# Performance work log

Measured on AMD Instinct MI355X. Metric: run time of the kernel, lower is better.

Reference implementation:

```python
import jax, jax.numpy as jnp
import numpy as np

MAX_M = 16
B, H, N_LEN = 16, 256, 4096


def _ref_dft_np(n, h):
    a = np.arange(n)
    M = np.exp(-2j * np.pi * np.outer(a, a) / n)  # (n, n) complex
    M = np.broadcast_to(M, (h, n, n))
    return np.ascontiguousarray(np.stack([M.real, M.imag], axis=-1)).astype(np.float32)


def setup_inputs() -> dict:
    key = jax.random.key(0)
    k1, k2 = jax.random.split(key)
    x_real = jax.random.normal(k1, (B, H, N_LEN), dtype=jnp.float32)
    x_imag = jax.random.normal(k2, (B, H, N_LEN), dtype=jnp.float32)
    # Learned DFT matrices are initialized to the exact reference DFT matrices
    # (learn_additive=False path in the torch module).
    return {
        "x_real": x_real,
        "x_imag": x_imag,
        "mat_2": jnp.asarray(_ref_dft_np(2, H)),
        "mat_4": jnp.asarray(_ref_dft_np(4, H)),
        "mat_8": jnp.asarray(_ref_dft_np(8, H)),
        "mat_16": jnp.asarray(_ref_dft_np(16, H)),
        "N": N_LEN,
    }


def _twiddle(n, m):
    na = jnp.arange(n)[:, None]
    ma = jnp.arange(m)[None, :]
    return jnp.exp((-2j * jnp.pi / (n * m)) * (na * ma).astype(jnp.float32))  # (n, m)


def _cooley_tukey(k, n, m, mats):
    # k: (..., n*m) complex; FFT of length n*m along last dim.
    k = k.reshape(k.shape[:-1] + (m, n))  # '... (m n) -> ... m n'
    # n m-length DFTs along rows: mats[m] is (H, m, m), broadcasts over leading dims.
    k_f = jnp.einsum('...mo,...on->...mn', mats[m], k)
    twi = _twiddle(n, m).astype(k_f.dtype)  # (n, m)
    k_f = jnp.einsum('nm,...mn->...nm', twi, k_f)  # transpose + twiddle
    if n <= MAX_M:
        k_f = jnp.einsum('...no,...om->...nm', mats[n], k_f)
    else:
        k_f = jnp.moveaxis(k_f, -1, -3)  # '... h n m -> ... m h n'
        k_f = _cooley_tukey(k_f, n // MAX_M, MAX_M, mats)
        k_f = jnp.moveaxis(k_f, -3, -1)  # '... m h n -> ... h n m'
    return k_f.reshape(k_f.shape[:-2] + (k_f.shape[-2] * k_f.shape[-1],))


def reference(x_real, x_imag, mat_2, mat_4, mat_8, mat_16, N):
    x = x_real + 1j * x_imag  # (B, H, N) complex64
    mats = {p: (mm[..., 0] + 1j * mm[..., 1])
            for p, mm in ((2, mat_2), (4, mat_4), (8, mat_8), (16, mat_16))}
    out = _cooley_tukey(x, N // MAX_M, MAX_M, mats)  # (B, H, N) complex
    # view_as_real representation of the complex FFT output
    return jnp.stack([out.real, out.imag], axis=-1)  # (B, H, N, 2)
```

## Files before the change

kernel.cpp:

```cpp
#include <hip/hip_runtime.h>
#include <stdint.h>

typedef _Float16 f16x8 __attribute__((ext_vector_type(8)));
typedef float    f32x4 __attribute__((ext_vector_type(4)));

union FragU { unsigned u[4]; f16x8 h; };

__device__ __forceinline__ unsigned pkh(float a, float b) {
    return __builtin_bit_cast(unsigned, __builtin_amdgcn_cvt_pkrtz(a, b));
}

#define MFMA(A, B, C) __builtin_amdgcn_mfma_f32_16x16x32_f16((A).h, (B).h, (C), 0, 0, 0)

#define K1 (-1.5339807878856412e-03f)
#define K2 (-2.4543692606170259e-02f)

__global__ __launch_bounds__(256) void fft4096_mfma(
    const float* __restrict__ xre, const float* __restrict__ xim,
    const float* __restrict__ mat16, float* __restrict__ out, int H)
{
    __shared__ __align__(16) unsigned char smem[33024];

    const int t = threadIdx.x;
    const int w = t >> 6;
    const int l = t & 63;
    const int g = l >> 4;
    const int c = l & 15;
    const int bh = blockIdx.x;
    const int h  = bh % H;
    const size_t base = (size_t)bh * 4096;

    const float* Mb = mat16 + (size_t)h * 512 + (size_t)c * 32 + g * 8;
    const float4 mf0 = *(const float4*)Mb;
    const float4 mf1 = *(const float4*)(Mb + 4);
    const unsigned mrA = pkh(mf0.x, mf0.z), mrB = pkh(mf1.x, mf1.z);
    const unsigned miA = pkh(mf0.y, mf0.w), miB = pkh(mf1.y, mf1.w);
    const unsigned nmiA = miA ^ 0x80008000u, nmiB = miB ^ 0x80008000u;

    FragU Afrag;
    Afrag.u[0] = mrA; Afrag.u[1] = mrB; Afrag.u[2] = miA; Afrag.u[3] = miB;
    FragU BMr;
    BMr.u[0] = mrA; BMr.u[1] = mrB; BMr.u[2] = nmiA; BMr.u[3] = nmiB;
    FragU BMi;
    BMi.u[0] = miA; BMi.u[1] = miB; BMi.u[2] = mrA; BMi.u[3] = mrB;

    const f32x4 zero = {0.f, 0.f, 0.f, 0.f};

    f32x4 s1r[4], s1i[4];
#pragma unroll
    for (int p = 0; p < 4; ++p) {
        const int col = (4 * w + p) * 16 + c;
        float xr[4], xi[4];
#pragma unroll
        for (int jj = 0; jj < 4; ++jj) {
            xr[jj] = xre[base + (size_t)((4 * g + jj) * 256 + col)];
            xi[jj] = xim[base + (size_t)((4 * g + jj) * 256 + col)];
        }
        const unsigned rp0 = pkh(xr[0], xr[1]), rp1 = pkh(xr[2], xr[3]);
        const unsigned ip0 = pkh(xi[0], xi[1]), ip1 = pkh(xi[2], xi[3]);
        const unsigned np0 = pkh(-xi[0], -xi[1]), np1 = pkh(-xi[2], -xi[3]);
        FragU Br; Br.u[0] = rp0; Br.u[1] = rp1; Br.u[2] = np0; Br.u[3] = np1;
        FragU Bi; Bi.u[0] = ip0; Bi.u[1] = ip1; Bi.u[2] = rp0; Bi.u[3] = rp1;
        s1r[p] = MFMA(Afrag, Br, zero);
        s1i[p] = MFMA(Afrag, Bi, zero);
    }
#pragma unroll
    for (int p = 0; p < 4; ++p) {
        const int j = (4 * w + p) * 16 + c;
        float sb, cb, ss, cs;
        __sincosf(K1 * (float)(j * 4 * g), &sb, &cb);
        __sincosf(K1 * (float)j, &ss, &cs);
#pragma unroll
        for (int reg = 0; reg < 4; ++reg) {
            const float yr = s1r[p][reg], yi = s1i[p][reg];
            s1r[p][reg] = yr * cb - yi * sb;
            s1i[p][reg] = yr * sb + yi * cb;
            const float nc = cb * cs - sb * ss;
            const float ns = cb * ss + sb * cs;
            cb = nc; sb = ns;
        }
    }
#pragma unroll
    for (int reg = 0; reg < 4; ++reg) {
        const int m1 = 4 * g + reg;
        const int half = m1 * 256 + c * 16 + 4 * ((w ^ (c >> 2) ^ reg) & 3);
        uint2 vr, vi;
        vr.x = pkh(s1r[0][reg], s1r[1][reg]); vr.y = pkh(s1r[2][reg], s1r[3][reg]);
        vi.x = pkh(s1i[0][reg], s1i[1][reg]); vi.y = pkh(s1i[2][reg], s1i[3][reg]);
        *(uint2*)(smem + half * 2)        = vr;
        *(uint2*)(smem + 8192 + half * 2) = vi;
    }
    __syncthreads();

    f32x4 s2r[4], s2i[4];
#pragma unroll
    for (int p = 0; p < 4; ++p) {
        const int m1 = 4 * w + p;
        const int half = m1 * 256 + c * 16 + 4 * ((g ^ (c >> 2) ^ p) & 3);
        const uint2 rp = *(const uint2*)(smem + half * 2);
        const uint2 ip = *(const uint2*)(smem + 8192 + half * 2);
        FragU Br; Br.u[0] = rp.x; Br.u[1] = rp.y;
        Br.u[2] = ip.x ^ 0x80008000u; Br.u[3] = ip.y ^ 0x80008000u;
        FragU Bi; Bi.u[0] = ip.x; Bi.u[1] = ip.y; Bi.u[2] = rp.x; Bi.u[3] = rp.y;
        s2r[p] = MFMA(Afrag, Br, zero);
        s2i[p] = MFMA(Afrag, Bi, zero);
    }
    float twc[4], tws[4];
    {
        float sb, cb, ss, cs;
        __sincosf(K2 * (float)(c * 4 * g), &sb, &cb);
        __sincosf(K2 * (float)c, &ss, &cs);
#pragma unroll
        for (int reg = 0; reg < 4; ++reg) {
            twc[reg] = cb; tws[reg] = sb;
            const float nc = cb * cs - sb * ss;
            const float ns = cb * ss + sb * cs;
            cb = nc; sb = ns;
        }
    }
#pragma unroll
    for (int p = 0; p < 4; ++p) {
#pragma unroll
        for (int reg = 0; reg < 4; ++reg) {
            const float yr = s2r[p][reg], yi = s2i[p][reg];
            s2r[p][reg] = yr * twc[reg] - yi * tws[reg];
            s2i[p][reg] = yr * tws[reg] + yi * twc[reg];
        }
    }
#pragma unroll
    for (int reg = 0; reg < 4; ++reg) {
        const int m2 = 4 * g + reg;
        const int half = m2 * 256 + c * 16 + 4 * ((w ^ (c >> 2) ^ reg) & 3);
        uint2 vr, vi;
        vr.x = pkh(s2r[0][reg], s2r[1][reg]); vr.y = pkh(s2r[2][reg], s2r[3][reg]);
        vi.x = pkh(s2i[0][reg], s2i[1][reg]); vi.y = pkh(s2i[2][reg], s2i[3][reg]);
        *(uint2*)(smem + 16384 + half * 2) = vr;
        *(uint2*)(smem + 24576 + half * 2) = vi;
    }
    __syncthreads();

    FragU Aup[4];
#pragma unroll
    for (int p = 0; p < 4; ++p) {
        unsigned short hr[4], hi[4];
#pragma unroll
        for (int jj = 0; jj < 4; ++jj) {
            const int o3 = 4 * g + jj;
            const int half = c * 256 + o3 * 16 + 4 * ((w ^ g ^ (c & 3)) & 3) + p;
            hr[jj] = *(const unsigned short*)(smem + 16384 + half * 2);
            hi[jj] = *(const unsigned short*)(smem + 24576 + half * 2);
        }
        Aup[p].u[0] = (unsigned)hr[0] | ((unsigned)hr[1] << 16);
        Aup[p].u[1] = (unsigned)hr[2] | ((unsigned)hr[3] << 16);
        Aup[p].u[2] = (unsigned)hi[0] | ((unsigned)hi[1] << 16);
        Aup[p].u[3] = (unsigned)hi[2] | ((unsigned)hi[3] << 16);
    }
    __syncthreads();

    f32x4 vR[4], vI[4];
#pragma unroll
    for (int p = 0; p < 4; ++p) {
        vR[p] = MFMA(Aup[p], BMr, zero);
        vI[p] = MFMA(Aup[p], BMi, zero);
    }
#pragma unroll
    for (int reg = 0; reg < 4; ++reg) {
        const int fidx = c * 258 + (4 * g + reg) * 16 + 4 * w;
        float4 a, b;
        a.x = vR[0][reg]; a.y = vI[0][reg]; a.z = vR[1][reg]; a.w = vI[1][reg];
        b.x = vR[2][reg]; b.y = vI[2][reg]; b.z = vR[3][reg]; b.w = vI[3][reg];
        *(float4*)(smem + (size_t)fidx * 8)      = a;
        *(float4*)(smem + (size_t)fidx * 8 + 16) = b;
    }
    __syncthreads();

    float2* __restrict__ og = (float2*)out;
#pragma unroll
    for (int jr = 0; jr < 16; ++jr) {
        const float2 v = *(const float2*)(smem + (size_t)(jr * 258 + t) * 8);
        og[base + (size_t)(jr * 256 + t)] = v;
    }
}

extern "C" void kernel_launch(void* const* d_in, const int* in_sizes, int n_in,
                              void* d_out, int out_size, void* d_ws, size_t ws_size,
                              hipStream_t stream)
{
    const float* xre = (const float*)d_in[0];
    const float* xim = (const float*)d_in[1];
    const float* m16 = (const float*)d_in[5];
    const int H  = in_sizes[5] / 512;
    const int BH = in_sizes[0] / 4096;
    fft4096_mfma<<<dim3(BH), dim3(256), 0, stream>>>(
        xre, xim, m16, (float*)d_out, H);
}
```

Before: 48.25 us.

## Write FFT output directly from registers and vectorize stage-3 LDS fragment loads

The stage-2 results are now scattered to LDS as individual fp16 values with an XOR swizzle, so stage 3 can gather its A fragments with two 8-byte loads instead of sixteen 2-byte loads. The final LDS staging pass for the output, along with two barriers, is removed. Each lane now stores its results straight to global memory as 32-byte float4 pairs. This trades more LDS store instructions and less coalesced global writes (contiguous 32-byte chunks per lane) for fewer LDS reads and fewer synchronisations.

```diff
diff --git a/kernel.cpp b/kernel.cpp
--- a/kernel.cpp
+++ b/kernel.cpp
@@ -9,6 +9,9 @@
 __device__ __forceinline__ unsigned pkh(float a, float b) {
     return __builtin_bit_cast(unsigned, __builtin_amdgcn_cvt_pkrtz(a, b));
 }
+__device__ __forceinline__ unsigned short h16(float a) {
+    return __builtin_bit_cast(unsigned short, (_Float16)a);
+}
 
 #define MFMA(A, B, C) __builtin_amdgcn_mfma_f32_16x16x32_f16((A).h, (B).h, (C), 0, 0, 0)
 
@@ -19,7 +22,7 @@
     const float* __restrict__ xre, const float* __restrict__ xim,
     const float* __restrict__ mat16, float* __restrict__ out, int H)
 {
-    __shared__ __align__(16) unsigned char smem[33024];
+    __shared__ __align__(16) unsigned char smem[32768];
 
     const int t = threadIdx.x;
     const int w = t >> 6;
@@ -130,32 +133,27 @@
 #pragma unroll
     for (int reg = 0; reg < 4; ++reg) {
         const int m2 = 4 * g + reg;
-        const int half = m2 * 256 + c * 16 + 4 * ((w ^ (c >> 2) ^ reg) & 3);
-        uint2 vr, vi;
-        vr.x = pkh(s2r[0][reg], s2r[1][reg]); vr.y = pkh(s2r[2][reg], s2r[3][reg]);
-        vi.x = pkh(s2i[0][reg], s2i[1][reg]); vi.y = pkh(s2i[2][reg], s2i[3][reg]);
-        *(uint2*)(smem + 16384 + half * 2) = vr;
-        *(uint2*)(smem + 24576 + half * 2) = vi;
+#pragma unroll
+        for (int p = 0; p < 4; ++p) {
+            const int spos = (((4 * w + p) * 16 + c) ^ (g << 4)) ^ (reg << 2);
+            const int half = m2 * 256 + spos;
+            *(unsigned short*)(smem + 16384 + half * 2) = h16(s2r[p][reg]);
+            *(unsigned short*)(smem + 24576 + half * 2) = h16(s2i[p][reg]);
+        }
     }
     __syncthreads();
 
     FragU Aup[4];
 #pragma unroll
     for (int p = 0; p < 4; ++p) {
-        unsigned short hr[4], hi[4];
-#pragma unroll
-        for (int jj = 0; jj < 4; ++jj) {
-            const int o3 = 4 * g + jj;
-            const int half = c * 256 + o3 * 16 + 4 * ((w ^ g ^ (c & 3)) & 3) + p;
-            hr[jj] = *(const unsigned short*)(smem + 16384 + half * 2);
-            hi[jj] = *(const unsigned short*)(smem + 24576 + half * 2);
-        }
-        Aup[p].u[0] = (unsigned)hr[0] | ((unsigned)hr[1] << 16);
-        Aup[p].u[1] = (unsigned)hr[2] | ((unsigned)hr[3] << 16);
-        Aup[p].u[2] = (unsigned)hi[0] | ((unsigned)hi[1] << 16);
-        Aup[p].u[3] = (unsigned)hi[2] | ((unsigned)hi[3] << 16);
+        const int spos = ((((4 * w + p) * 16 + 4 * g) ^ (((c >> 2) & 3) << 4))
+                          ^ ((c & 3) << 2));
+        const int half = c * 256 + spos;
+        const uint2 hr = *(const uint2*)(smem + 16384 + half * 2);
+        const uint2 hi = *(const uint2*)(smem + 24576 + half * 2);
+        Aup[p].u[0] = hr.x; Aup[p].u[1] = hr.y;
+        Aup[p].u[2] = hi.x; Aup[p].u[3] = hi.y;
     }
-    __syncthreads();
 
     f32x4 vR[4], vI[4];
 #pragma unroll
@@ -163,22 +161,16 @@
         vR[p] = MFMA(Aup[p], BMr, zero);
         vI[p] = MFMA(Aup[p], BMi, zero);
     }
+
+    float2* __restrict__ og = (float2*)out;
 #pragma unroll
     for (int reg = 0; reg < 4; ++reg) {
-        const int fidx = c * 258 + (4 * g + reg) * 16 + 4 * w;
+        const size_t k0 = base + (size_t)(c * 256 + (4 * g + reg) * 16 + 4 * w);
         float4 a, b;
         a.x = vR[0][reg]; a.y = vI[0][reg]; a.z = vR[1][reg]; a.w = vI[1][reg];
         b.x = vR[2][reg]; b.y = vI[2][reg]; b.z = vR[3][reg]; b.w = vI[3][reg];
-        *(float4*)(smem + (size_t)fidx * 8)      = a;
-        *(float4*)(smem + (size_t)fidx * 8 + 16) = b;
-    }
-    __syncthreads();
-
-    float2* __restrict__ og = (float2*)out;
-#pragma unroll
-    for (int jr = 0; jr < 16; ++jr) {
-        const float2 v = *(const float2*)(smem + (size_t)(jr * 258 + t) * 8);
-        og[base + (size_t)(jr * 256 + t)] = v;
+        *(float4*)&og[k0]     = a;
+        *(float4*)&og[k0 + 2] = b;
     }
 }
 
```

After: 58.98 us. 1.22x slower.
